# Performance work log

Hardware: AMD Instinct MI355X
Metric: run time of the kernel (lower is better)

The kernel has to match this reference:

```python
import jax, jax.numpy as jnp
import numpy as np

B, S, IN, D, HID, H, K, YD = 4, 2048, 64, 128, 400, 4, 20, 4
WHICH_OUT = 0
ALPHAS = jnp.array([0.05, 0.06, 0.08, 0.1, 0.12, 0.14, 0.15, 0.17, 0.19, 0.2,
                    0.21, 0.23, 0.25, 0.3, 0.35, 0.38, 0.4, 0.45], dtype=jnp.float32)  # 18 alphas


def _mlp(x, W1, b1, W2, b2, W3, b3, W4, b4):
    # FcModel encoder: in -> 400 -> 400 -> 400 -> out, ReLU hidden, linear head
    h = jax.nn.relu(x @ W1 + b1)
    h = jax.nn.relu(h @ W2 + b2)
    h = jax.nn.relu(h @ W3 + b3)
    return h @ W4 + b4


def _ln(x, g, b):
    mu = jnp.mean(x, axis=-1, keepdims=True)
    var = jnp.var(x, axis=-1, keepdims=True)
    return (x - mu) * jax.lax.rsqrt(var + 1e-5) * g + b


def setup_inputs() -> dict:
    key = jax.random.key(0)
    ks = jax.random.split(key, 16)
    w = lambda k, shape: 0.05 * jax.random.normal(k, shape, dtype=jnp.float32)
    return {
        'X_ctx_true': jax.random.normal(ks[0], (B, S, IN), dtype=jnp.float32),
        'X_ctx_sim':  jax.random.normal(ks[1], (B, S, IN), dtype=jnp.float32),
        'errors':     jax.random.normal(ks[2], (B, S, YD), dtype=jnp.float32),
        'y':          jax.random.normal(ks[3], (B, S, YD), dtype=jnp.float32),
        'y_pred':     jax.random.normal(ks[4], (B, S, YD), dtype=jnp.float32),
        'W1': w(ks[5], (IN, HID)),  'b1': jnp.zeros((HID,), jnp.float32),
        'W2': w(ks[6], (HID, HID)), 'b2': jnp.zeros((HID,), jnp.float32),
        'W3': w(ks[7], (HID, HID)), 'b3': jnp.zeros((HID,), jnp.float32),
        'W4': w(ks[8], (HID, D)),   'b4': jnp.zeros((D,), jnp.float32),
        'Wq': w(ks[9], (D, H * D)), 'bq': jnp.zeros((H * D,), jnp.float32),
        'Wk': w(ks[10], (D, H * D)), 'bk': jnp.zeros((H * D,), jnp.float32),
        'g_q': jnp.ones((D,), jnp.float32), 'beta_q': jnp.zeros((D,), jnp.float32),
        'g_k': jnp.ones((D,), jnp.float32), 'beta_k': jnp.zeros((D,), jnp.float32),
    }


def reference(X_ctx_true, X_ctx_sim, errors, y, y_pred,
              W1, b1, W2, b2, W3, b3, W4, b4,
              Wq, bq, Wk, bk, g_q, beta_q, g_k, beta_k):
    err_w = errors[..., WHICH_OUT]                      # [B,S]
    enc_true = _mlp(X_ctx_true, W1, b1, W2, b2, W3, b3, W4, b4)  # [B,S,D]
    enc_sim = _mlp(X_ctx_sim, W1, b1, W2, b2, W3, b3, W4, b4)    # [B,S,D]

    # Hopfield association: LayerNorm on state (query) and stored (key) patterns,
    # per-head projection to hidden_size=D, scaled dot product, diag mask, softmax.
    q = (_ln(enc_true, g_q, beta_q) @ Wq + bq).reshape(B, S, H, D)
    k = (_ln(enc_sim, g_k, beta_k) @ Wk + bk).reshape(B, S, H, D)
    scores = jnp.einsum('bshd,bmhd->bhsm', q, k) / jnp.sqrt(jnp.float32(D))
    diag = jnp.eye(S, dtype=bool)
    scores = jnp.where(diag[None, None], -jnp.inf, scores)
    assoc = jax.nn.softmax(scores, axis=-1)             # [B,H,S,M]

    # topk sampling of memory slots, gather corresponding errors
    _, idx = jax.lax.top_k(assoc, K)                    # [B,H,S,K]
    sel = err_w[jnp.arange(B)[:, None, None, None], idx]  # [B,H,S,K]

    # quantiles over samples for all alphas at once (torch.quantile = linear interp)
    betas = ALPHAS / 2.0
    q_low = jnp.quantile(sel, betas, axis=-1)           # [A,B,H,S]
    q_high = jnp.quantile(sel, 1.0 - ALPHAS + betas, axis=-1)  # [A,B,H,S]

    yp = y_pred[..., WHICH_OUT]                         # [B,S]
    y_low = q_low + yp[None, :, None, :]                # [A,B,H,S]
    y_high = q_high + yp[None, :, None, :]

    # mean-quantile MSE score, per head then averaged
    mean_err = jnp.concatenate([q_low, q_high], axis=0).mean(axis=0)  # [B,H,S]
    pred_adj = mean_err + yp[:, None, :]                # [B,H,S]
    y_true = y[..., WHICH_OUT]                          # [B,S]
    scores_per_head = jnp.mean((y_true[:, None, :] - pred_adj) ** 2, axis=(0, 2))  # [H]
    score = jnp.mean(scores_per_head)

    to_out = lambda a: jnp.transpose(a, (2, 1, 0, 3))[..., None]  # [A,B,H,S]->[H,B,A,S,1]
    return (score, y, y_pred, to_out(y_low), to_out(y_high),
            errors[..., WHICH_OUT:WHICH_OUT + 1], to_out(q_low), to_out(q_high))
```

## Files before the change

kernel.cpp:

```cpp
#include <hip/hip_runtime.h>
#include <hip/hip_bf16.h>
#include <math.h>


#define SS 2048
#define ROWS 16
#define AST 400

typedef short short8v __attribute__((ext_vector_type(8)));
typedef float float4v __attribute__((ext_vector_type(4)));
typedef float float2v __attribute__((ext_vector_type(2)));

__constant__ float c_alphas[18] = {0.05f,0.06f,0.08f,0.1f,0.12f,0.14f,0.15f,0.17f,
                                   0.19f,0.2f,0.21f,0.23f,0.25f,0.3f,0.35f,0.38f,0.4f,0.45f};

#define OFF_Y      1
#define OFF_YPRED  32769
#define OFF_YLOW   65537ll
#define OFF_YHIGH  655361ll
#define OFF_ERR    1245185ll
#define OFF_QLOW   1253377ll
#define OFF_QHIGH  1843201ll

__device__ inline short f2bf_s(float f) {
    __hip_bfloat16 h = __float2bfloat16(f);
    return __builtin_bit_cast(short, h);
}
__device__ inline unsigned mono(float f) {
    unsigned u = __builtin_bit_cast(unsigned, f);
    return (u & 0x80000000u) ? ~u : (u | 0x80000000u);
}
__device__ inline unsigned umin_(unsigned a, unsigned b) { return a < b ? a : b; }
__device__ inline unsigned umax_(unsigned a, unsigned b) { return a > b ? a : b; }


template<int IN_W, int NCC>
__device__ __forceinline__ void mlp_layer_acc(
    const float* __restrict__ W, const float* __restrict__ act,
    const int w, const int t, float (&acc)[ROWS][2])
{
    int jm[2];
    #pragma unroll
    for (int cc = 0; cc < NCC; ++cc) {
        const int j = w*128 + cc*64 + t;
        jm[cc] = (j < 400) ? j : 399;
    }
    #pragma unroll
    for (int r = 0; r < ROWS; ++r)
        #pragma unroll
        for (int cc = 0; cc < NCC; ++cc) acc[r][cc] = 0.f;

    #pragma unroll 2
    for (int i4 = 0; i4 < IN_W/4; ++i4) {
        float wv[4][2];
        #pragma unroll
        for (int jj = 0; jj < 4; ++jj)
            #pragma unroll
            for (int cc = 0; cc < NCC; ++cc)
                wv[jj][cc] = W[(i4*4 + jj)*400 + jm[cc]];
        #pragma unroll
        for (int r = 0; r < ROWS; ++r) {
            const float4v xv = *(const float4v*)(act + r*AST + i4*4);
            #pragma unroll
            for (int jj = 0; jj < 4; ++jj)
                #pragma unroll
                for (int cc = 0; cc < NCC; ++cc)
                    acc[r][cc] = fmaf(xv[jj], wv[jj][cc], acc[r][cc]);
        }
    }
}

__device__ __forceinline__ void mlp_layer_store(
    const float* __restrict__ b, float* __restrict__ act,
    const int w, const int t, const int ncc, const float (&acc)[ROWS][2])
{
    #pragma unroll
    for (int cc = 0; cc < 2; ++cc) {
        const int j = w*128 + cc*64 + t;
        if (cc < ncc && j < 400) {
            const float bv = b[j];
            #pragma unroll
            for (int r = 0; r < ROWS; ++r)
                act[r*AST + j] = fmaxf(acc[r][cc] + bv, 0.f);
        }
    }
}

__global__ __launch_bounds__(256, 4) void k_mlp(
    const float* __restrict__ Xt, const float* __restrict__ Xs,
    const float* __restrict__ W1, const float* __restrict__ b1,
    const float* __restrict__ W2, const float* __restrict__ b2,
    const float* __restrict__ W3, const float* __restrict__ b3,
    const float* __restrict__ W4, const float* __restrict__ b4,
    const float* __restrict__ Wq, const float* __restrict__ bq,
    const float* __restrict__ Wk, const float* __restrict__ bk,
    const float* __restrict__ g_q, const float* __restrict__ beta_q,
    const float* __restrict__ g_k, const float* __restrict__ beta_k,
    float* __restrict__ qf, float* __restrict__ kf,
    __hip_bfloat16* __restrict__ khi)
{
    __shared__ float act[ROWS*AST];

    const int tid  = threadIdx.x;
    const int t    = tid & 63;
    const int w    = tid >> 6;
    const int bi   = blockIdx.x;
    const int half = bi >> 9;
    const int rbase = (bi & 511) * ROWS;
    const float* X = half ? Xs : Xt;

    #pragma unroll
    for (int u = 0; u < (ROWS*64)/256; ++u) {
        const int e = u*256 + tid;
        act[(e >> 6)*AST + (e & 63)] = X[(size_t)rbase*64 + e];
    }
    __syncthreads();

    float acc[ROWS][2];
    const int ncc = (w == 3) ? 1 : 2;

    if (w == 3) mlp_layer_acc<64,1>(W1, act, w, t, acc);
    else        mlp_layer_acc<64,2>(W1, act, w, t, acc);
    __syncthreads();
    mlp_layer_store(b1, act, w, t, ncc, acc);
    __syncthreads();

    if (w == 3) mlp_layer_acc<400,1>(W2, act, w, t, acc);
    else        mlp_layer_acc<400,2>(W2, act, w, t, acc);
    __syncthreads();
    mlp_layer_store(b2, act, w, t, ncc, acc);
    __syncthreads();

    if (w == 3) mlp_layer_acc<400,1>(W3, act, w, t, acc);
    else        mlp_layer_acc<400,2>(W3, act, w, t, acc);
    __syncthreads();
    mlp_layer_store(b3, act, w, t, ncc, acc);
    __syncthreads();

    float2v a4[4];
    #pragma unroll
    for (int rr = 0; rr < 4; ++rr) a4[rr] = (float2v){0.f, 0.f};
    #pragma unroll 2
    for (int i4 = 0; i4 < 100; ++i4) {
        float wv0[4], wv1[4];
        #pragma unroll
        for (int jj = 0; jj < 4; ++jj) {
            wv0[jj] = W4[(i4*4 + jj)*128 + t];
            wv1[jj] = W4[(i4*4 + jj)*128 + 64 + t];
        }
        #pragma unroll
        for (int rr = 0; rr < 4; ++rr) {
            const float4v xv = *(const float4v*)(act + (w*4 + rr)*AST + i4*4);
            #pragma unroll
            for (int jj = 0; jj < 4; ++jj) {
                a4[rr][0] = fmaf(xv[jj], wv0[jj], a4[rr][0]);
                a4[rr][1] = fmaf(xv[jj], wv1[jj], a4[rr][1]);
            }
        }
    }
    {
        const float b40 = b4[t], b41 = b4[64 + t];
        #pragma unroll
        for (int rr = 0; rr < 4; ++rr) { a4[rr][0] += b40; a4[rr][1] += b41; }
    }
    __syncthreads();

    {
        const float* g  = half ? g_k : g_q;
        const float* be = half ? beta_k : beta_q;
        const float gl0 = g[t],  gl1 = g[64 + t];
        const float bl0 = be[t], bl1 = be[64 + t];
        #pragma unroll
        for (int rr = 0; rr < 4; ++rr) {
            float s = a4[rr][0] + a4[rr][1];
            #pragma unroll
            for (int o = 32; o > 0; o >>= 1) s += __shfl_xor(s, o);
            const float mu = s * (1.f/128.f);
            const float d0 = a4[rr][0] - mu, d1 = a4[rr][1] - mu;
            float vs = d0*d0 + d1*d1;
            #pragma unroll
            for (int o = 32; o > 0; o >>= 1) vs += __shfl_xor(vs, o);
            const float rstd = rsqrtf(vs * (1.f/128.f) + 1e-5f);
            act[(w*4 + rr)*128 + t]      = d0*rstd*gl0 + bl0;
            act[(w*4 + rr)*128 + 64 + t] = d1*rstd*gl1 + bl1;
        }
    }
    __syncthreads();

    {
        const float* Wp = half ? Wk : Wq;
        const float* bp = half ? bk : bq;
        float* of = half ? kf : qf;

        float accp[ROWS][2];
        #pragma unroll
        for (int r = 0; r < ROWS; ++r) { accp[r][0] = 0.f; accp[r][1] = 0.f; }
        #pragma unroll 2
        for (int i4 = 0; i4 < 32; ++i4) {
            float wv[4][2];
            #pragma unroll
            for (int jj = 0; jj < 4; ++jj)
                #pragma unroll
                for (int cc = 0; cc < 2; ++cc)
                    wv[jj][cc] = Wp[(i4*4 + jj)*512 + w*128 + cc*64 + t];
            #pragma unroll
            for (int r = 0; r < ROWS; ++r) {
                const float4v xv = *(const float4v*)(act + r*128 + i4*4);
                #pragma unroll
                for (int jj = 0; jj < 4; ++jj)
                    #pragma unroll
                    for (int cc = 0; cc < 2; ++cc)
                        accp[r][cc] = fmaf(xv[jj], wv[jj][cc], accp[r][cc]);
            }
        }

        float bpv[2];
        bpv[0] = bp[w*128 + t];
        bpv[1] = bp[w*128 + 64 + t];
        #pragma unroll
        for (int r = 0; r < ROWS; ++r) {
            const int gidx = rbase + r;
            const int bb = gidx >> 11, s = gidx & 2047;
            const int T = s >> 4, m16s = s & 15;
            #pragma unroll
            for (int cc = 0; cc < 2; ++cc) {
                const int j  = w*128 + cc*64 + t;
                const int hh = j >> 7, d = j & 127;
                const float v = accp[r][cc] + bpv[cc];
                const size_t dst = ((size_t)(bb*4 + hh)*2048 + s)*128 + d;
                of[dst] = v;
                if (half) {
                    const int ks = d >> 5, qd = (d & 31) >> 3, jj = d & 7;
                    const size_t so = (size_t)(bb*4 + hh)*262144
                                    + (size_t)T*2048 + ks*512 + qd*128 + m16s*8 + jj;
                    khi[so] = __float2bfloat16(v);
                }
            }
        }
    }
}

__global__ __launch_bounds__(256, 4) void k_scan(
    const float* __restrict__ qf, const __hip_bfloat16* __restrict__ khi,
    unsigned* __restrict__ wsk)
{
    __shared__ unsigned kd[64*97];

    const int tid   = threadIdx.x;
    const int stile = blockIdx.x;
    const int hb    = blockIdx.y;
    const int mq    = blockIdx.z;

    const int lane = tid & 63;
    const int w    = tid >> 6;
    const int m16  = lane & 15;
    const int quad = lane >> 4;

    const size_t slab = (size_t)hb * 2048;
    const __hip_bfloat16* slabp = khi + (size_t)hb * 262144;

    const int sg_my = stile*64 + w*16 + m16;

    short8v bq_[4];
    {
        const float* qp = qf + (slab + sg_my)*128 + quad*8;
        #pragma unroll
        for (int ks = 0; ks < 4; ++ks) {
            const float4 x0 = *(const float4*)(qp + ks*32);
            const float4 x1 = *(const float4*)(qp + ks*32 + 4);
            short8v tt;
            tt[0]=f2bf_s(x0.x); tt[1]=f2bf_s(x0.y); tt[2]=f2bf_s(x0.z); tt[3]=f2bf_s(x0.w);
            tt[4]=f2bf_s(x1.x); tt[5]=f2bf_s(x1.y); tt[6]=f2bf_s(x1.z); tt[7]=f2bf_s(x1.w);
            bq_[ks] = tt;
        }
    }

    unsigned KA[12], KB[12];
    #pragma unroll
    for (int n = 0; n < 12; ++n) { KA[n] = 0u; KB[n] = 0u; }

    #pragma unroll 1
    for (int cti = 0; cti < 32; ++cti) {
        const int T = mq*32 + cti;
        const __hip_bfloat16* kp = slabp + (size_t)T*2048 + lane*8;
        float4v acc = (float4v){0.f,0.f,0.f,0.f};
        #pragma unroll
        for (int ks = 0; ks < 4; ++ks) {
            const short8v ka = *(const short8v*)(kp + ks*512);
            acc = __builtin_amdgcn_mfma_f32_16x16x32_bf16(ka, bq_[ks], acc, 0, 0, 0);
        }
        const int cb = T*16 + quad*4;
        #pragma unroll
        for (int ph = 0; ph < 2; ++ph) {
            {
                const int m = cb + ph;
                unsigned key = (mono(acc[ph]) & 0xFFFFF800u) | (unsigned)m;
                key = (m == sg_my) ? 0u : key;
                KA[0] = umax_(KA[0], key);
                #pragma unroll
                for (int i = 0; i < 11; ++i) {
                    const unsigned a = KA[i], c = KA[i+1];
                    KA[i]   = umin_(a, c);
                    KA[i+1] = umax_(a, c);
                }
            }
            {
                const int m = cb + 2 + ph;
                unsigned key = (mono(acc[2+ph]) & 0xFFFFF800u) | (unsigned)m;
                key = (m == sg_my) ? 0u : key;
                KB[0] = umax_(KB[0], key);
                #pragma unroll
                for (int i = 0; i < 11; ++i) {
                    const unsigned a = KB[i], c = KB[i+1];
                    KB[i]   = umin_(a, c);
                    KB[i+1] = umax_(a, c);
                }
            }
        }
    }

    const int rr = w*16 + m16;
    #pragma unroll
    for (int n = 0; n < 12; ++n) {
        kd[rr*97 + (quad*2 + 0)*12 + n] = KA[11 - n];
        kd[rr*97 + (quad*2 + 1)*12 + n] = KB[11 - n];
    }
    __syncthreads();

    if (quad == 0) {
        const unsigned* R = &kd[rr*97];
        int q0=0,q1=0,q2=0,q3=0,q4=0,q5=0,q6=0,q7=0;
        const size_t base = (size_t)hb*2048 + stile*64 + rr;
        #pragma unroll 1
        for (int n = 0; n < 24; ++n) {
            const unsigned h0 = (q0<12)?R[  0+q0]:0u;
            const unsigned h1 = (q1<12)?R[ 12+q1]:0u;
            const unsigned h2 = (q2<12)?R[ 24+q2]:0u;
            const unsigned h3 = (q3<12)?R[ 36+q3]:0u;
            const unsigned h4 = (q4<12)?R[ 48+q4]:0u;
            const unsigned h5 = (q5<12)?R[ 60+q5]:0u;
            const unsigned h6 = (q6<12)?R[ 72+q6]:0u;
            const unsigned h7 = (q7<12)?R[ 84+q7]:0u;
            unsigned bv = h0; int bs = 0;
            if (h1 > bv) { bv = h1; bs = 1; }
            if (h2 > bv) { bv = h2; bs = 2; }
            if (h3 > bv) { bv = h3; bs = 3; }
            if (h4 > bv) { bv = h4; bs = 4; }
            if (h5 > bv) { bv = h5; bs = 5; }
            if (h6 > bv) { bv = h6; bs = 6; }
            if (h7 > bv) { bv = h7; bs = 7; }
            q0 += (bs==0); q1 += (bs==1); q2 += (bs==2); q3 += (bs==3);
            q4 += (bs==4); q5 += (bs==5); q6 += (bs==6); q7 += (bs==7);
            wsk[(size_t)(mq*24 + n)*32768 + base] = bv;
        }
    }
}

__global__ __launch_bounds__(256, 4) void k_select(
    const float* __restrict__ qf, const float* __restrict__ kf,
    const unsigned* __restrict__ wsk,
    const float* __restrict__ errors, const float* __restrict__ y,
    const float* __restrict__ y_pred,
    float* __restrict__ out, float* __restrict__ hacc)
{
    __shared__ unsigned kd[64*4*25];
    __shared__ unsigned short cb[64*33];
    __shared__ float es[64*33];
    __shared__ float ebuf[64*21];

    const int tid   = threadIdx.x;
    const int stile = blockIdx.x;
    const int hb    = blockIdx.y;
    const int b     = hb >> 2;
    const int h     = hb & 3;

    const int lane = tid & 63;
    const int w    = tid >> 6;
    const int m16  = lane & 15;
    const int quad = lane >> 4;
    const int rr   = w*16 + m16;
    const int sg   = stile*64 + rr;

    const size_t base = (size_t)hb*2048 + sg;
    #pragma unroll 1
    for (int n = 0; n < 24; ++n)
        kd[(rr*4 + quad)*25 + n] = wsk[(size_t)(quad*24 + n)*32768 + base];
    __syncthreads();

    if (quad == 0) {
        const unsigned* L0 = &kd[(rr*4 + 0)*25];
        const unsigned* L1 = &kd[(rr*4 + 1)*25];
        const unsigned* L2 = &kd[(rr*4 + 2)*25];
        const unsigned* L3 = &kd[(rr*4 + 3)*25];
        int p0 = 0, p1 = 0, p2 = 0, p3 = 0;
        #pragma unroll 1
        for (int n = 0; n < 32; ++n) {
            const unsigned h0 = (p0 < 24) ? L0[p0] : 0u;
            const unsigned h1 = (p1 < 24) ? L1[p1] : 0u;
            const unsigned h2 = (p2 < 24) ? L2[p2] : 0u;
            const unsigned h3 = (p3 < 24) ? L3[p3] : 0u;
            unsigned bv = h0; int bs = 0;
            if (h1 > bv) { bv = h1; bs = 1; }
            if (h2 > bv) { bv = h2; bs = 2; }
            if (h3 > bv) { bv = h3; bs = 3; }
            if (bs == 0) ++p0; else if (bs == 1) ++p1; else if (bs == 2) ++p2; else ++p3;
            cb[rr*33 + n] = (unsigned short)(bv & 0x7FFu);
        }
    }
    __syncthreads();

    const size_t slab = (size_t)hb * 2048;
    const float* qrow_p = qf + (slab + sg)*128;
    float4 qseg[8];
    #pragma unroll
    for (int u = 0; u < 8; ++u)
        qseg[u] = *(const float4*)(qrow_p + quad*4 + u*16);
    const float* kslab = kf + slab*128;
    #pragma unroll 1
    for (int n = 0; n < 32; ++n) {
        const int col = cb[rr*33 + n];
        const float* kc = kslab + (size_t)col*128 + quad*4;
        float2v s01 = (float2v){0.f, 0.f}, s23 = (float2v){0.f, 0.f};
        #pragma unroll
        for (int u = 0; u < 8; ++u) {
            const float4 kv = *(const float4*)(kc + u*16);
            s01 = __builtin_elementwise_fma((float2v){qseg[u].x, qseg[u].y},
                                            (float2v){kv.x, kv.y}, s01);
            s23 = __builtin_elementwise_fma((float2v){qseg[u].z, qseg[u].w},
                                            (float2v){kv.z, kv.w}, s23);
        }
        float v = (s01[0] + s01[1]) + (s23[0] + s23[1]);
        v += __shfl_xor(v, 16);
        v += __shfl_xor(v, 32);
        if (quad == 0) es[rr*33 + n] = v;
    }

    float sq = 0.f;
    if (quad == 0) {
        float* e = &ebuf[rr*21];
        #pragma unroll 1
        for (int k = 0; k < 20; ++k) {
            float best = -INFINITY; int bc = 4096, bj = 0;
            #pragma unroll 1
            for (int j = 0; j < 32; ++j) {
                const float v = es[rr*33 + j];
                const int c = cb[rr*33 + j];
                if (v > best || (v == best && c < bc)) { best = v; bc = c; bj = j; }
            }
            es[rr*33 + bj] = -INFINITY;
            e[k] = errors[((size_t)(b*SS + bc))*4];
        }
        #pragma unroll 1
        for (int a = 1; a < 20; ++a) {
            const float v = e[a];
            int n = a;
            while (n > 0 && e[n-1] > v) { e[n] = e[n-1]; --n; }
            e[n] = v;
        }
        const float yp = y_pred[((size_t)(b*SS + sg))*4];
        const float yt = y[((size_t)(b*SS + sg))*4];
        float msum = 0.f;
        const size_t obase = ((size_t)(h*4 + b)*18)*2048 + sg;
        #pragma unroll 1
        for (int a = 0; a < 18; ++a) {
            const float alpha = c_alphas[a];
            const float beta  = 0.5f*alpha;
            const float pl = beta * 19.f;
            const int   il = (int)pl;
            const float fl = pl - (float)il;
            const float ql = e[il]*(1.f-fl) + e[il+1]*fl;
            const float qq = (1.f - alpha) + beta;
            const float ph = qq * 19.f;
            const int   ih = (int)ph;
            const float fh = ph - (float)ih;
            const float qh = e[ih]*(1.f-fh) + e[ih+1]*fh;
            msum += ql + qh;
            const size_t oidx = obase + (size_t)a*2048;
            out[OFF_YLOW  + oidx] = ql + yp;
            out[OFF_YHIGH + oidx] = qh + yp;
            out[OFF_QLOW  + oidx] = ql;
            out[OFF_QHIGH + oidx] = qh;
        }
        const float me = msum * (1.f/36.f);
        const float dd = yt - (me + yp);
        sq = dd*dd;
    }
    #pragma unroll
    for (int o = 32; o > 0; o >>= 1) sq += __shfl_xor(sq, o);
    if (lane == 0) atomicAdd(&hacc[h], sq);
}

__global__ void k_init(float* __restrict__ hacc) {
    if (threadIdx.x < 4) hacc[threadIdx.x] = 0.f;
}

__global__ __launch_bounds__(256) void k_finalize(
    const float* __restrict__ y, const float* __restrict__ y_pred,
    const float* __restrict__ errors, const float* __restrict__ hacc,
    float* __restrict__ out)
{
    const int i = blockIdx.x*256 + threadIdx.x;
    if (i == 0)
        out[0] = (hacc[0]+hacc[1]+hacc[2]+hacc[3]) * (1.f/32768.f);
    if (i < 32768)      out[OFF_Y + i] = y[i];
    else if (i < 65536) out[OFF_YPRED + (i - 32768)] = y_pred[i - 32768];
    else if (i < 73728) { const int j = i - 65536; out[OFF_ERR + j] = errors[(size_t)j*4]; }
}

extern "C" void kernel_launch(void* const* d_in, const int* in_sizes, int n_in,
                              void* d_out, int out_size, void* d_ws, size_t ws_size,
                              hipStream_t stream)
{
    const float* Xt     = (const float*)d_in[0];
    const float* Xs     = (const float*)d_in[1];
    const float* errors = (const float*)d_in[2];
    const float* y      = (const float*)d_in[3];
    const float* y_pred = (const float*)d_in[4];
    const float* W1 = (const float*)d_in[5];   const float* b1 = (const float*)d_in[6];
    const float* W2 = (const float*)d_in[7];   const float* b2 = (const float*)d_in[8];
    const float* W3 = (const float*)d_in[9];   const float* b3 = (const float*)d_in[10];
    const float* W4 = (const float*)d_in[11];  const float* b4 = (const float*)d_in[12];
    const float* Wq = (const float*)d_in[13];  const float* bq = (const float*)d_in[14];
    const float* Wk = (const float*)d_in[15];  const float* bk = (const float*)d_in[16];
    const float* g_q    = (const float*)d_in[17];
    const float* beta_q = (const float*)d_in[18];
    const float* g_k    = (const float*)d_in[19];
    const float* beta_k = (const float*)d_in[20];

    float* out  = (float*)d_out;
    char*  base = (char*)d_ws;
    const size_t SLAB = (size_t)16*2048*128;
    float* hacc = (float*)base;
    float* qf   = (float*)(base + 256);
    float* kf   = qf + SLAB;
    __hip_bfloat16* khi = (__hip_bfloat16*)(kf + SLAB);
    unsigned* wsk = (unsigned*)(khi + SLAB);

    k_init<<<1, 64, 0, stream>>>(hacc);
    k_mlp<<<1024, 256, 0, stream>>>(Xt, Xs, W1,b1,W2,b2,W3,b3,W4,b4,
                                    Wq,bq,Wk,bk,g_q,beta_q,g_k,beta_k,
                                    qf, kf, khi);
    k_scan<<<dim3(32,16,4), 256, 0, stream>>>(qf, khi, wsk);
    k_select<<<dim3(32,16), 256, 0, stream>>>(qf, kf, wsk, errors, y, y_pred, out, hacc);
    k_finalize<<<288, 256, 0, stream>>>(y, y_pred, errors, hacc, out);
}
```

Measured before the change: 610.7 us.

## Halve MLP rows per block, rotate column slices, register-resident top-k selection

The MLP kernel now processes 8 rows per block instead of 16, launches twice as many blocks, and raises the launch-bounds occupancy target from 4 to 6 blocks. It also rotates which wave owns the short last column slice by block index, to spread the idle-lane imbalance across waves. In k_select, the 20-step top-k selection is fully unrolled over register arrays instead of repeatedly scanning shared memory, and the error gathers are batched after selection. Each block now reuses each weight load across half as many rows, the top-k change raises register pressure, and k_select's occupancy hint is lowered to 2.

```diff
diff --git a/kernel.cpp b/kernel.cpp
--- a/kernel.cpp
+++ b/kernel.cpp
@@ -4,7 +4,7 @@
 
 
 #define SS 2048
-#define ROWS 16
+#define ROWS 8
 #define AST 400
 
 typedef short short8v __attribute__((ext_vector_type(8)));
@@ -37,14 +37,8 @@
 template<int IN_W, int NCC>
 __device__ __forceinline__ void mlp_layer_acc(
     const float* __restrict__ W, const float* __restrict__ act,
-    const int w, const int t, float (&acc)[ROWS][2])
-{
-    int jm[2];
-    #pragma unroll
-    for (int cc = 0; cc < NCC; ++cc) {
-        const int j = w*128 + cc*64 + t;
-        jm[cc] = (j < 400) ? j : 399;
-    }
+    const int jm0, const int jm1, float (&acc)[ROWS][2])
+{
     #pragma unroll
     for (int r = 0; r < ROWS; ++r)
         #pragma unroll
@@ -54,10 +48,10 @@
     for (int i4 = 0; i4 < IN_W/4; ++i4) {
         float wv[4][2];
         #pragma unroll
-        for (int jj = 0; jj < 4; ++jj)
-            #pragma unroll
-            for (int cc = 0; cc < NCC; ++cc)
-                wv[jj][cc] = W[(i4*4 + jj)*400 + jm[cc]];
+        for (int jj = 0; jj < 4; ++jj) {
+            wv[jj][0] = W[(i4*4 + jj)*400 + jm0];
+            if (NCC > 1) wv[jj][1] = W[(i4*4 + jj)*400 + jm1];
+        }
         #pragma unroll
         for (int r = 0; r < ROWS; ++r) {
             const float4v xv = *(const float4v*)(act + r*AST + i4*4);
@@ -72,21 +66,24 @@
 
 __device__ __forceinline__ void mlp_layer_store(
     const float* __restrict__ b, float* __restrict__ act,
-    const int w, const int t, const int ncc, const float (&acc)[ROWS][2])
-{
-    #pragma unroll
-    for (int cc = 0; cc < 2; ++cc) {
-        const int j = w*128 + cc*64 + t;
-        if (cc < ncc && j < 400) {
-            const float bv = b[j];
-            #pragma unroll
-            for (int r = 0; r < ROWS; ++r)
-                act[r*AST + j] = fmaxf(acc[r][cc] + bv, 0.f);
-        }
-    }
-}
-
-__global__ __launch_bounds__(256, 4) void k_mlp(
+    const int jm0, const int jm1, const bool on0, const bool on1,
+    const float (&acc)[ROWS][2])
+{
+    if (on0) {
+        const float bv = b[jm0];
+        #pragma unroll
+        for (int r = 0; r < ROWS; ++r)
+            act[r*AST + jm0] = fmaxf(acc[r][0] + bv, 0.f);
+    }
+    if (on1) {
+        const float bv = b[jm1];
+        #pragma unroll
+        for (int r = 0; r < ROWS; ++r)
+            act[r*AST + jm1] = fmaxf(acc[r][1] + bv, 0.f);
+    }
+}
+
+__global__ __launch_bounds__(256, 6) void k_mlp(
     const float* __restrict__ Xt, const float* __restrict__ Xs,
     const float* __restrict__ W1, const float* __restrict__ b1,
     const float* __restrict__ W2, const float* __restrict__ b2,
@@ -105,9 +102,18 @@
     const int t    = tid & 63;
     const int w    = tid >> 6;
     const int bi   = blockIdx.x;
-    const int half = bi >> 9;
-    const int rbase = (bi & 511) * ROWS;
+    const int half = bi >> 10;
+    const int rbase = (bi & 1023) * ROWS;
     const float* X = half ? Xs : Xt;
+
+    const int sl  = (w + bi) & 3;
+    const int j0  = sl*128 + t;
+    const int j1  = sl*128 + 64 + t;
+    const int jm0 = (j0 < 400) ? j0 : 399;
+    const int jm1 = (j1 < 400) ? j1 : 399;
+    const bool on0 = (j0 < 400);
+    const bool on1 = (j1 < 400);
+    const bool s3  = (sl == 3);
 
     #pragma unroll
     for (int u = 0; u < (ROWS*64)/256; ++u) {
@@ -117,29 +123,28 @@
     __syncthreads();
 
     float acc[ROWS][2];
-    const int ncc = (w == 3) ? 1 : 2;
-
-    if (w == 3) mlp_layer_acc<64,1>(W1, act, w, t, acc);
-    else        mlp_layer_acc<64,2>(W1, act, w, t, acc);
-    __syncthreads();
-    mlp_layer_store(b1, act, w, t, ncc, acc);
-    __syncthreads();
-
-    if (w == 3) mlp_layer_acc<400,1>(W2, act, w, t, acc);
-    else        mlp_layer_acc<400,2>(W2, act, w, t, acc);
-    __syncthreads();
-    mlp_layer_store(b2, act, w, t, ncc, acc);
-    __syncthreads();
-
-    if (w == 3) mlp_layer_acc<400,1>(W3, act, w, t, acc);
-    else        mlp_layer_acc<400,2>(W3, act, w, t, acc);
-    __syncthreads();
-    mlp_layer_store(b3, act, w, t, ncc, acc);
-    __syncthreads();
-
-    float2v a4[4];
-    #pragma unroll
-    for (int rr = 0; rr < 4; ++rr) a4[rr] = (float2v){0.f, 0.f};
+
+    if (s3) mlp_layer_acc<64,1>(W1, act, jm0, jm1, acc);
+    else    mlp_layer_acc<64,2>(W1, act, jm0, jm1, acc);
+    __syncthreads();
+    mlp_layer_store(b1, act, jm0, jm1, on0, on1 && !s3, acc);
+    __syncthreads();
+
+    if (s3) mlp_layer_acc<400,1>(W2, act, jm0, jm1, acc);
+    else    mlp_layer_acc<400,2>(W2, act, jm0, jm1, acc);
+    __syncthreads();
+    mlp_layer_store(b2, act, jm0, jm1, on0, on1 && !s3, acc);
+    __syncthreads();
+
+    if (s3) mlp_layer_acc<400,1>(W3, act, jm0, jm1, acc);
+    else    mlp_layer_acc<400,2>(W3, act, jm0, jm1, acc);
+    __syncthreads();
+    mlp_layer_store(b3, act, jm0, jm1, on0, on1 && !s3, acc);
+    __syncthreads();
+
+    float2v a4[2];
+    #pragma unroll
+    for (int rr = 0; rr < 2; ++rr) a4[rr] = (float2v){0.f, 0.f};
     #pragma unroll 2
     for (int i4 = 0; i4 < 100; ++i4) {
         float wv0[4], wv1[4];
@@ -149,8 +154,8 @@
             wv1[jj] = W4[(i4*4 + jj)*128 + 64 + t];
         }
         #pragma unroll
-        for (int rr = 0; rr < 4; ++rr) {
-            const float4v xv = *(const float4v*)(act + (w*4 + rr)*AST + i4*4);
+        for (int rr = 0; rr < 2; ++rr) {
+            const float4v xv = *(const float4v*)(act + (w*2 + rr)*AST + i4*4);
             #pragma unroll
             for (int jj = 0; jj < 4; ++jj) {
                 a4[rr][0] = fmaf(xv[jj], wv0[jj], a4[rr][0]);
@@ -161,7 +166,7 @@
     {
         const float b40 = b4[t], b41 = b4[64 + t];
         #pragma unroll
-        for (int rr = 0; rr < 4; ++rr) { a4[rr][0] += b40; a4[rr][1] += b41; }
+        for (int rr = 0; rr < 2; ++rr) { a4[rr][0] += b40; a4[rr][1] += b41; }
     }
     __syncthreads();
 
@@ -171,7 +176,7 @@
         const float gl0 = g[t],  gl1 = g[64 + t];
         const float bl0 = be[t], bl1 = be[64 + t];
         #pragma unroll
-        for (int rr = 0; rr < 4; ++rr) {
+        for (int rr = 0; rr < 2; ++rr) {
             float s = a4[rr][0] + a4[rr][1];
             #pragma unroll
             for (int o = 32; o > 0; o >>= 1) s += __shfl_xor(s, o);
@@ -181,8 +186,8 @@
             #pragma unroll
             for (int o = 32; o > 0; o >>= 1) vs += __shfl_xor(vs, o);
             const float rstd = rsqrtf(vs * (1.f/128.f) + 1e-5f);
-            act[(w*4 + rr)*128 + t]      = d0*rstd*gl0 + bl0;
-            act[(w*4 + rr)*128 + 64 + t] = d1*rstd*gl1 + bl1;
+            act[(w*2 + rr)*128 + t]      = d0*rstd*gl0 + bl0;
+            act[(w*2 + rr)*128 + 64 + t] = d1*rstd*gl1 + bl1;
         }
     }
     __syncthreads();
@@ -199,39 +204,37 @@
         for (int i4 = 0; i4 < 32; ++i4) {
             float wv[4][2];
             #pragma unroll
-            for (int jj = 0; jj < 4; ++jj)
-                #pragma unroll
-                for (int cc = 0; cc < 2; ++cc)
-                    wv[jj][cc] = Wp[(i4*4 + jj)*512 + w*128 + cc*64 + t];
+            for (int jj = 0; jj < 4; ++jj) {
+                wv[jj][0] = Wp[(i4*4 + jj)*512 + j0];
+                wv[jj][1] = Wp[(i4*4 + jj)*512 + j1];
+            }
             #pragma unroll
             for (int r = 0; r < ROWS; ++r) {
                 const float4v xv = *(const float4v*)(act + r*128 + i4*4);
                 #pragma unroll
-                for (int jj = 0; jj < 4; ++jj)
-                    #pragma unroll
-                    for (int cc = 0; cc < 2; ++cc)
-                        accp[r][cc] = fmaf(xv[jj], wv[jj][cc], accp[r][cc]);
-            }
-        }
-
-        float bpv[2];
-        bpv[0] = bp[w*128 + t];
-        bpv[1] = bp[w*128 + 64 + t];
+                for (int jj = 0; jj < 4; ++jj) {
+                    accp[r][0] = fmaf(xv[jj], wv[jj][0], accp[r][0]);
+                    accp[r][1] = fmaf(xv[jj], wv[jj][1], accp[r][1]);
+                }
+            }
+        }
+
+        const float bp0 = bp[j0], bp1 = bp[j1];
         #pragma unroll
         for (int r = 0; r < ROWS; ++r) {
             const int gidx = rbase + r;
-            const int bb = gidx >> 11, s = gidx & 2047;
+            const int bB = gidx >> 11, s = gidx & 2047;
             const int T = s >> 4, m16s = s & 15;
             #pragma unroll
             for (int cc = 0; cc < 2; ++cc) {
-                const int j  = w*128 + cc*64 + t;
+                const int j  = cc ? j1 : j0;
                 const int hh = j >> 7, d = j & 127;
-                const float v = accp[r][cc] + bpv[cc];
-                const size_t dst = ((size_t)(bb*4 + hh)*2048 + s)*128 + d;
+                const float v = (cc ? accp[r][1] : accp[r][0]) + (cc ? bp1 : bp0);
+                const size_t dst = ((size_t)(bB*4 + hh)*2048 + s)*128 + d;
                 of[dst] = v;
                 if (half) {
                     const int ks = d >> 5, qd = (d & 31) >> 3, jj = d & 7;
-                    const size_t so = (size_t)(bb*4 + hh)*262144
+                    const size_t so = (size_t)(bB*4 + hh)*262144
                                     + (size_t)T*2048 + ks*512 + qd*128 + m16s*8 + jj;
                     khi[so] = __float2bfloat16(v);
                 }
@@ -356,7 +359,7 @@
     }
 }
 
-__global__ __launch_bounds__(256, 4) void k_select(
+__global__ __launch_bounds__(256, 2) void k_select(
     const float* __restrict__ qf, const float* __restrict__ kf,
     const unsigned* __restrict__ wsk,
     const float* __restrict__ errors, const float* __restrict__ y,
@@ -437,19 +440,32 @@
 
     float sq = 0.f;
     if (quad == 0) {
-        float* e = &ebuf[rr*21];
-        #pragma unroll 1
+        float rv[32]; int cvv[32];
+        #pragma unroll
+        for (int j = 0; j < 32; ++j) {
+            rv[j]  = es[rr*33 + j];
+            cvv[j] = (int)cb[rr*33 + j];
+        }
+        int bcs[20];
+        #pragma unroll
         for (int k = 0; k < 20; ++k) {
             float best = -INFINITY; int bc = 4096, bj = 0;
-            #pragma unroll 1
+            #pragma unroll
             for (int j = 0; j < 32; ++j) {
-                const float v = es[rr*33 + j];
-                const int c = cb[rr*33 + j];
-                if (v > best || (v == best && c < bc)) { best = v; bc = c; bj = j; }
-            }
-            es[rr*33 + bj] = -INFINITY;
-            e[k] = errors[((size_t)(b*SS + bc))*4];
-        }
+                const bool tk = (rv[j] > best) || (rv[j] == best && cvv[j] < bc);
+                best = tk ? rv[j]  : best;
+                bc   = tk ? cvv[j] : bc;
+                bj   = tk ? j      : bj;
+            }
+            #pragma unroll
+            for (int j = 0; j < 32; ++j)
+                rv[j] = (j == bj) ? -INFINITY : rv[j];
+            bcs[k] = bc;
+        }
+        float* e = &ebuf[rr*21];
+        #pragma unroll
+        for (int k = 0; k < 20; ++k)
+            e[k] = errors[((size_t)(b*SS + bcs[k]))*4];
         #pragma unroll 1
         for (int a = 1; a < 20; ++a) {
             const float v = e[a];
@@ -537,7 +553,7 @@
     unsigned* wsk = (unsigned*)(khi + SLAB);
 
     k_init<<<1, 64, 0, stream>>>(hacc);
-    k_mlp<<<1024, 256, 0, stream>>>(Xt, Xs, W1,b1,W2,b2,W3,b3,W4,b4,
+    k_mlp<<<2048, 256, 0, stream>>>(Xt, Xs, W1,b1,W2,b2,W3,b3,W4,b4,
                                     Wq,bq,Wk,bk,g_q,beta_q,g_k,beta_k,
                                     qf, kf, khi);
     k_scan<<<dim3(32,16,4), 256, 0, stream>>>(qf, khi, wsk);
```

Result: slower. 707.8 us (+15.9%).
